# Kernel tuning notes

Measured on AMD Instinct MI355X. Metric: run time of the kernel, lower is better.

## Reference

```python
import jax, jax.numpy as jnp
import numpy as np

BATCH = 1024
A = 128  # image height
B = 128  # image width (must equal A for the original matmul chain to type-check)
N = 64   # attention grid size
H = 1024 # h_dim


def setup_inputs() -> dict:
    key = jax.random.key(0)
    k0, k1, k2, k3 = jax.random.split(key, 4)
    x = jax.random.normal(k0, (BATCH, A * B), dtype=jnp.float32)
    x_hat = jax.random.normal(k1, (BATCH, A * B), dtype=jnp.float32)
    h = jax.random.normal(k2, (BATCH, H), dtype=jnp.float32)
    W_read_w = jax.random.normal(k3, (5, H), dtype=jnp.float32) * 0.02
    W_read_b = jnp.zeros((5,), dtype=jnp.float32)
    return {"x": x, "x_hat": x_hat, "h": h, "W_read_w": W_read_w, "W_read_b": W_read_b}


def _compute_filterbanks(params):
    # params: (5,) from W_read(h)[0]
    gt_X, gt_Y, log_var, log_dt = params[0], params[1], params[2], params[3]
    var = jnp.exp(log_var + 1e-8)
    # .item() in the original detaches these from the autograd graph
    g_X = jax.lax.stop_gradient((A + 1) * (gt_X + 1) / 2)
    g_Y = jax.lax.stop_gradient((B + 1) * (gt_Y + 1) / 2)
    d = jax.lax.stop_gradient(jnp.exp(log_dt) * (max(A, B) - 1) / (N - 1))
    # linspace(g + (-N/2-0.5)d, g + (N-1-N/2-0.5)d, N) == g + (i - N/2 - 0.5)*d
    idx = jnp.arange(N, dtype=jnp.float32) - N / 2 - 0.5  # (N,)
    mu_X = g_X + idx * d  # (N,)
    mu_Y = g_Y + idx * d  # (N,)
    a = jnp.arange(A, dtype=jnp.float32)
    b = jnp.arange(B, dtype=jnp.float32)
    F_X = jnp.exp(-((a[None, :] - mu_X[:, None]) ** 2) / (2 * var))  # (N, A)
    F_Y = jnp.exp(-((b[None, :] - mu_Y[:, None]) ** 2) / (2 * var))  # (N, B)
    # NOTE: original normalizes by the GLOBAL sum, not per-row
    F_X = F_X / jnp.sum(F_X)
    F_Y = F_Y / jnp.sum(F_Y)
    return F_X, F_Y


def reference(x, x_hat, h, W_read_w, W_read_b):
    # params from FIRST batch element, shared across the whole batch (as in original)
    params = (h @ W_read_w.T + W_read_b)[0]  # (5,)
    gamma = jnp.exp(params[4])
    F_X, F_Y = _compute_filterbanks(params)  # (N,A), (N,B)

    xi = x.reshape(-1, A, B)
    xh = x_hat.reshape(-1, A, B)

    def filt(z):  # gamma * F_Y @ z @ F_X.T  -> (batch, N, N)
        t = jnp.einsum('na,kab->knb', F_Y, z)      # (batch, N, B)
        return gamma * jnp.einsum('knb,mb->knm', t, F_X)

    x_filt = filt(xi).reshape(-1, N * N)
    x_hat_filt = filt(xh).reshape(-1, N * N)
    return jnp.concatenate([x_filt, x_hat_filt], axis=1)  # (batch, 2*N*N)
```

## Files before the change

### kernel.cpp

```cpp
#include <hip/hip_runtime.h>
#include <math.h>

#define AB 128
#define NN 64
#define HD 1024

#define SFZ 256.0f
#define SFF 64.0f
#define DESCALE (1.0f / 1048576.0f)

typedef _Float16 half8 __attribute__((ext_vector_type(8)));
typedef float f32x4 __attribute__((ext_vector_type(4)));
typedef unsigned u32x4 __attribute__((ext_vector_type(4)));


__device__ __forceinline__ float wave_reduce(float v) {
  v += __shfl_down(v, 32);
  v += __shfl_down(v, 16);
  v += __shfl_down(v, 8);
  v += __shfl_down(v, 4);
  v += __shfl_down(v, 2);
  v += __shfl_down(v, 1);
  return v;
}

__global__ __launch_bounds__(1024) void fb_setup(
    const float* __restrict__ h, const float* __restrict__ Ww,
    const float* __restrict__ Wb, void* __restrict__ wsv) {
  __shared__ float redp[16][5];
  __shared__ float reds[16][2];
  __shared__ float sc[5];
  __shared__ float ssum[2];
  const int tid = threadIdx.x;
  const int lane = tid & 63;
  const int wv = tid >> 6;

  const float hv = h[tid];
  float p[5];
#pragma unroll
  for (int j = 0; j < 5; ++j) p[j] = hv * Ww[j * HD + tid];
#pragma unroll
  for (int j = 0; j < 5; ++j) {
    float r = wave_reduce(p[j]);
    if (lane == 0) redp[wv][j] = r;
  }
  __syncthreads();
  if (tid < 5) {
    float s = Wb[tid];
#pragma unroll
    for (int w = 0; w < 16; ++w) s += redp[w][tid];
    sc[tid] = s;
  }
  __syncthreads();

  const float gt_X = sc[0], gt_Y = sc[1], log_var = sc[2], log_dt = sc[3];
  const float var = expf(log_var + 1e-8f);
  const float g_X = (129.0f * (gt_X + 1.0f)) / 2.0f;
  const float g_Y = (129.0f * (gt_Y + 1.0f)) / 2.0f;
  const float d = (expf(log_dt) * 127.0f) / 63.0f;
  const float twovar = 2.0f * var;

  float fyv[8], fxv[8];
  float sY = 0.f, sX = 0.f;
#pragma unroll
  for (int c = 0; c < 8; ++c) {
    const int idx = tid + 1024 * c;
    const int n = idx >> 7;
    const int col = idx & 127;
    const float idxn = (float)n - 32.5f;
    const float muX = g_X + idxn * d;
    const float muY = g_Y + idxn * d;
    const float dx = (float)col - muX;
    const float dy = (float)col - muY;
    const float fx = expf(-(dx * dx) / twovar);
    const float fy = expf(-(dy * dy) / twovar);
    fyv[c] = fy;
    fxv[c] = fx;
    sY += fy;
    sX += fx;
  }
  {
    float rY = wave_reduce(sY);
    float rX = wave_reduce(sX);
    if (lane == 0) { reds[wv][0] = rY; reds[wv][1] = rX; }
  }
  __syncthreads();
  if (tid < 2) {
    float s = 0.f;
#pragma unroll
    for (int w = 0; w < 16; ++w) s += reds[w][tid];
    ssum[tid] = s;
  }
  __syncthreads();
  const float invY = 1.0f / ssum[0];
  const float invX = 1.0f / ssum[1];

  _Float16* FXhi = (_Float16*)wsv;
  _Float16* FXlo = FXhi + NN * AB;
  _Float16* FYhi = FXhi + 2 * NN * AB;
  _Float16* FYlo = FXhi + 3 * NN * AB;

#pragma unroll
  for (int c = 0; c < 8; ++c) {
    const int idx = tid + 1024 * c;
    const float vy = fyv[c] * invY * SFF;
    const float vx = fxv[c] * invX * SFF;
    const _Float16 yh = (_Float16)vy;
    const _Float16 xh2 = (_Float16)vx;
    FYhi[idx] = yh;
    FYlo[idx] = (_Float16)(vy - (float)yh);
    FXhi[idx] = xh2;
    FXlo[idx] = (_Float16)(vx - (float)xh2);
  }
  if (tid == 0) ((float*)wsv)[2 * NN * AB] = expf(sc[4]) * DESCALE;
}

__device__ __forceinline__ void split8(const f32x4 z0, const f32x4 z1,
                                       float s, half8& hi, half8& lo) {
#pragma unroll
  for (int e = 0; e < 8; ++e) {
    const float q = (e < 4 ? z0[e] : z1[e - 4]) * s;
    const _Float16 hh = (_Float16)q;
    hi[e] = hh;
    lo[e] = (_Float16)(q - (float)hh);
  }
}

__global__ __launch_bounds__(256) void fb_filt(
    const float* __restrict__ x, const float* __restrict__ xh,
    const void* __restrict__ wsv, float* __restrict__ out) {
  __shared__ unsigned S_lds[NN * 140];

  const int tid = threadIdx.x;
  const int lane = tid & 63;
  const int wv = tid >> 6;
  const int l15 = lane & 15;
  const int h4 = lane >> 4;
  const int bid = blockIdx.x;
  const int img = bid >> 1;
  const int which = bid & 1;
  const float* __restrict__ Z = (which ? xh : x) + (size_t)img * (AB * AB);
  const _Float16* __restrict__ FXhi = (const _Float16*)wsv;
  const _Float16* __restrict__ FXlo = FXhi + NN * AB;
  const _Float16* __restrict__ FYhi = FXhi + 2 * NN * AB;
  const _Float16* __restrict__ FYlo = FXhi + 3 * NN * AB;

  f32x4 acc[4][2];
#pragma unroll
  for (int mt = 0; mt < 4; ++mt)
#pragma unroll
    for (int j = 0; j < 2; ++j) acc[mt][j] = {0.f, 0.f, 0.f, 0.f};

#pragma unroll
  for (int ks = 0; ks < 4; ++ks) {
    half8 bhi[2], blo[2];
#pragma unroll
    for (int j = 0; j < 2; ++j) {
      const float* zp = Z + (32 * wv + 16 * j + l15) * AB + 32 * ks + 8 * h4;
      const f32x4 z0 = *(const f32x4*)zp;
      const f32x4 z1 = *(const f32x4*)(zp + 4);
      split8(z0, z1, SFZ, bhi[j], blo[j]);
    }
#pragma unroll
    for (int mt = 0; mt < 4; ++mt) {
      const int off = (16 * mt + l15) * AB + 32 * ks + 8 * h4;
      const half8 ahi = *(const half8*)(FXhi + off);
      const half8 alo = *(const half8*)(FXlo + off);
#pragma unroll
      for (int j = 0; j < 2; ++j) {
        acc[mt][j] = __builtin_amdgcn_mfma_f32_16x16x32_f16(ahi, bhi[j], acc[mt][j], 0, 0, 0);
        acc[mt][j] = __builtin_amdgcn_mfma_f32_16x16x32_f16(ahi, blo[j], acc[mt][j], 0, 0, 0);
        acc[mt][j] = __builtin_amdgcn_mfma_f32_16x16x32_f16(alo, bhi[j], acc[mt][j], 0, 0, 0);
      }
    }
  }

#pragma unroll
  for (int mt = 0; mt < 4; ++mt) {
#pragma unroll
    for (int j = 0; j < 2; ++j) {
      const int a = 32 * wv + 16 * j + l15;
#pragma unroll
      for (int r = 0; r < 4; ++r) {
        const float v = acc[mt][j][r];
        const _Float16 hh = (_Float16)v;
        const _Float16 ll = (_Float16)(v - (float)hh);
        const unsigned wpk =
            ((unsigned)__builtin_bit_cast(unsigned short, hh) << 16) |
            (unsigned)__builtin_bit_cast(unsigned short, ll);
        S_lds[(16 * mt + 4 * h4 + r) * 140 + a] = wpk;
      }
    }
  }
  __syncthreads();

  f32x4 acc2[4];
#pragma unroll
  for (int mt = 0; mt < 4; ++mt) acc2[mt] = {0.f, 0.f, 0.f, 0.f};

#pragma unroll
  for (int ks = 0; ks < 4; ++ks) {
    const int aoff = 32 * ks + 8 * h4;
    const int foff = (16 * wv + l15) * AB + aoff;
    const half8 ahi = *(const half8*)(FYhi + foff);
    const half8 alo = *(const half8*)(FYlo + foff);
#pragma unroll
    for (int mt = 0; mt < 4; ++mt) {
      const unsigned* sp = &S_lds[(16 * mt + l15) * 140 + aoff];
      const u32x4 w0 = *(const u32x4*)sp;
      const u32x4 w1 = *(const u32x4*)(sp + 4);
      u32x4 bhu, blu;
      bhu.x = __builtin_amdgcn_perm(w0.y, w0.x, 0x07060302u);
      blu.x = __builtin_amdgcn_perm(w0.y, w0.x, 0x05040100u);
      bhu.y = __builtin_amdgcn_perm(w0.w, w0.z, 0x07060302u);
      blu.y = __builtin_amdgcn_perm(w0.w, w0.z, 0x05040100u);
      bhu.z = __builtin_amdgcn_perm(w1.y, w1.x, 0x07060302u);
      blu.z = __builtin_amdgcn_perm(w1.y, w1.x, 0x05040100u);
      bhu.w = __builtin_amdgcn_perm(w1.w, w1.z, 0x07060302u);
      blu.w = __builtin_amdgcn_perm(w1.w, w1.z, 0x05040100u);
      const half8 bh = __builtin_bit_cast(half8, bhu);
      const half8 bl = __builtin_bit_cast(half8, blu);
      acc2[mt] = __builtin_amdgcn_mfma_f32_16x16x32_f16(ahi, bh, acc2[mt], 0, 0, 0);
      acc2[mt] = __builtin_amdgcn_mfma_f32_16x16x32_f16(ahi, bl, acc2[mt], 0, 0, 0);
      acc2[mt] = __builtin_amdgcn_mfma_f32_16x16x32_f16(alo, bh, acc2[mt], 0, 0, 0);
    }
  }

  const float gamma_eff = ((const float*)wsv)[2 * NN * AB];
  float* __restrict__ ob = out + (size_t)img * 8192 + which * 4096;
#pragma unroll
  for (int mt = 0; mt < 4; ++mt) {
#pragma unroll
    for (int r = 0; r < 4; ++r) {
      ob[(16 * wv + 4 * h4 + r) * 64 + 16 * mt + l15] = acc2[mt][r] * gamma_eff;
    }
  }
}

extern "C" void kernel_launch(void* const* d_in, const int* in_sizes, int n_in,
                              void* d_out, int out_size, void* d_ws, size_t ws_size,
                              hipStream_t stream) {
  const float* x = (const float*)d_in[0];
  const float* xh = (const float*)d_in[1];
  const float* h = (const float*)d_in[2];
  const float* Ww = (const float*)d_in[3];
  const float* Wb = (const float*)d_in[4];
  float* outp = (float*)d_out;

  fb_setup<<<1, 1024, 0, stream>>>(h, Ww, Wb, d_ws);
  fb_filt<<<2048, 256, 0, stream>>>(x, xh, (const void*)d_ws, outp);
}
```

Measured before the change: 195.2 us.

## Stage packed FX filterbank in swizzled LDS and prefetch image and FY operands

FX hi/lo halves are now packed into one 32-bit word per element in the workspace. Each block copies the packed array into an XOR-swizzled LDS buffer instead of every wave reading FX from global/L2 per k-step. Image loads are issued early and split around the LDS fill, FY fragments are preloaded into registers before the second GEMM, and stage-2 LDS reads are software-pipelined one tile ahead. The change adds a barrier and reuses the LDS buffer for both stages, raises register pressure with the launch_bounds occupancy hint, and relies on the swizzle to avoid bank conflicts that the old padding handled.

```diff
diff --git a/kernel.cpp b/kernel.cpp
--- a/kernel.cpp
+++ b/kernel.cpp
@@ -95,10 +95,9 @@
   const float invY = 1.0f / ssum[0];
   const float invX = 1.0f / ssum[1];
 
-  _Float16* FXhi = (_Float16*)wsv;
-  _Float16* FXlo = FXhi + NN * AB;
-  _Float16* FYhi = FXhi + 2 * NN * AB;
-  _Float16* FYlo = FXhi + 3 * NN * AB;
+  unsigned* FXp = (unsigned*)wsv;
+  _Float16* FYhi = (_Float16*)wsv + 2 * NN * AB;
+  _Float16* FYlo = FYhi + NN * AB;
 
 #pragma unroll
   for (int c = 0; c < 8; ++c) {
@@ -109,8 +108,9 @@
     const _Float16 xh2 = (_Float16)vx;
     FYhi[idx] = yh;
     FYlo[idx] = (_Float16)(vy - (float)yh);
-    FXhi[idx] = xh2;
-    FXlo[idx] = (_Float16)(vx - (float)xh2);
+    const _Float16 xl = (_Float16)(vx - (float)xh2);
+    FXp[idx] = ((unsigned)__builtin_bit_cast(unsigned short, xh2) << 16) |
+               (unsigned)__builtin_bit_cast(unsigned short, xl);
   }
   if (tid == 0) ((float*)wsv)[2 * NN * AB] = expf(sc[4]) * DESCALE;
 }
@@ -126,10 +126,25 @@
   }
 }
 
-__global__ __launch_bounds__(256) void fb_filt(
+__device__ __forceinline__ void unpack8(const u32x4 a0, const u32x4 a1,
+                                        half8& hi, half8& lo) {
+  u32x4 hu, lu;
+  hu.x = __builtin_amdgcn_perm(a0.y, a0.x, 0x07060302u);
+  lu.x = __builtin_amdgcn_perm(a0.y, a0.x, 0x05040100u);
+  hu.y = __builtin_amdgcn_perm(a0.w, a0.z, 0x07060302u);
+  lu.y = __builtin_amdgcn_perm(a0.w, a0.z, 0x05040100u);
+  hu.z = __builtin_amdgcn_perm(a1.y, a1.x, 0x07060302u);
+  lu.z = __builtin_amdgcn_perm(a1.y, a1.x, 0x05040100u);
+  hu.w = __builtin_amdgcn_perm(a1.w, a1.z, 0x07060302u);
+  lu.w = __builtin_amdgcn_perm(a1.w, a1.z, 0x05040100u);
+  hi = __builtin_bit_cast(half8, hu);
+  lo = __builtin_bit_cast(half8, lu);
+}
+
+__global__ __launch_bounds__(256, 4) void fb_filt(
     const float* __restrict__ x, const float* __restrict__ xh,
     const void* __restrict__ wsv, float* __restrict__ out) {
-  __shared__ unsigned S_lds[NN * 140];
+  __shared__ __align__(16) unsigned S_lds[NN * 128];
 
   const int tid = threadIdx.x;
   const int lane = tid & 63;
@@ -140,10 +155,44 @@
   const int img = bid >> 1;
   const int which = bid & 1;
   const float* __restrict__ Z = (which ? xh : x) + (size_t)img * (AB * AB);
-  const _Float16* __restrict__ FXhi = (const _Float16*)wsv;
-  const _Float16* __restrict__ FXlo = FXhi + NN * AB;
-  const _Float16* __restrict__ FYhi = FXhi + 2 * NN * AB;
-  const _Float16* __restrict__ FYlo = FXhi + 3 * NN * AB;
+  const unsigned* __restrict__ FXp = (const unsigned*)wsv;
+  const _Float16* __restrict__ FYhi = (const _Float16*)wsv + 2 * NN * AB;
+  const _Float16* __restrict__ FYlo = FYhi + NN * AB;
+  const float gamma_eff = ((const float*)wsv)[2 * NN * AB];
+
+  const float* __restrict__ zrow = Z + (32 * wv + l15) * AB + 8 * h4;
+  f32x4 z[4][4];
+#pragma unroll
+  for (int ks = 0; ks < 2; ++ks) {
+    const float* p0 = zrow + 32 * ks;
+    const float* p1 = zrow + 16 * AB + 32 * ks;
+    z[ks][0] = *(const f32x4*)p0;
+    z[ks][1] = *(const f32x4*)(p0 + 4);
+    z[ks][2] = *(const f32x4*)p1;
+    z[ks][3] = *(const f32x4*)(p1 + 4);
+  }
+  {
+    const int swc = 4 * ((tid >> 5) & 7);
+    const int colw = (tid * 4) & 127;
+    const int rbase = tid >> 5;
+#pragma unroll
+    for (int c = 0; c < 8; ++c) {
+      const u32x4 v = *(const u32x4*)(FXp + c * 1024 + tid * 4);
+      *(u32x4*)&S_lds[(c * 8 + rbase) * 128 + (colw ^ swc)] = v;
+    }
+  }
+  __syncthreads();
+
+#pragma unroll
+  for (int ks = 2; ks < 4; ++ks) {
+    const float* p0 = zrow + 32 * ks;
+    const float* p1 = zrow + 16 * AB + 32 * ks;
+    z[ks][0] = *(const f32x4*)p0;
+    z[ks][1] = *(const f32x4*)(p0 + 4);
+    z[ks][2] = *(const f32x4*)p1;
+    z[ks][3] = *(const f32x4*)(p1 + 4);
+  }
+  __builtin_amdgcn_sched_barrier(0);
 
   f32x4 acc[4][2];
 #pragma unroll
@@ -151,21 +200,20 @@
 #pragma unroll
     for (int j = 0; j < 2; ++j) acc[mt][j] = {0.f, 0.f, 0.f, 0.f};
 
+  const int sw1 = 4 * (l15 & 7);
 #pragma unroll
   for (int ks = 0; ks < 4; ++ks) {
     half8 bhi[2], blo[2];
-#pragma unroll
-    for (int j = 0; j < 2; ++j) {
-      const float* zp = Z + (32 * wv + 16 * j + l15) * AB + 32 * ks + 8 * h4;
-      const f32x4 z0 = *(const f32x4*)zp;
-      const f32x4 z1 = *(const f32x4*)(zp + 4);
-      split8(z0, z1, SFZ, bhi[j], blo[j]);
-    }
+    split8(z[ks][0], z[ks][1], SFZ, bhi[0], blo[0]);
+    split8(z[ks][2], z[ks][3], SFZ, bhi[1], blo[1]);
+    const int c0 = (32 * ks + 8 * h4) ^ sw1;
 #pragma unroll
     for (int mt = 0; mt < 4; ++mt) {
-      const int off = (16 * mt + l15) * AB + 32 * ks + 8 * h4;
-      const half8 ahi = *(const half8*)(FXhi + off);
-      const half8 alo = *(const half8*)(FXlo + off);
+      const int base = (16 * mt + l15) * 128;
+      const u32x4 a0 = *(const u32x4*)&S_lds[base + c0];
+      const u32x4 a1 = *(const u32x4*)&S_lds[base + (c0 ^ 4)];
+      half8 ahi, alo;
+      unpack8(a0, a1, ahi, alo);
 #pragma unroll
       for (int j = 0; j < 2; ++j) {
         acc[mt][j] = __builtin_amdgcn_mfma_f32_16x16x32_f16(ahi, bhi[j], acc[mt][j], 0, 0, 0);
@@ -174,6 +222,7 @@
       }
     }
   }
+  __syncthreads();
 
 #pragma unroll
   for (int mt = 0; mt < 4; ++mt) {
@@ -182,51 +231,55 @@
       const int a = 32 * wv + 16 * j + l15;
 #pragma unroll
       for (int r = 0; r < 4; ++r) {
+        const int row = 16 * mt + 4 * h4 + r;
         const float v = acc[mt][j][r];
         const _Float16 hh = (_Float16)v;
         const _Float16 ll = (_Float16)(v - (float)hh);
         const unsigned wpk =
             ((unsigned)__builtin_bit_cast(unsigned short, hh) << 16) |
             (unsigned)__builtin_bit_cast(unsigned short, ll);
-        S_lds[(16 * mt + 4 * h4 + r) * 140 + a] = wpk;
+        S_lds[row * 128 + ((a >> 2) * 4 ^ (4 * (row & 7))) + (a & 3)] = wpk;
       }
     }
   }
+
+  half8 fyh[4], fyl[4];
+#pragma unroll
+  for (int ks = 0; ks < 4; ++ks) {
+    const int foff = (16 * wv + l15) * AB + 32 * ks + 8 * h4;
+    fyh[ks] = *(const half8*)(FYhi + foff);
+    fyl[ks] = *(const half8*)(FYlo + foff);
+  }
+  __builtin_amdgcn_sched_barrier(0);
   __syncthreads();
 
   f32x4 acc2[4];
 #pragma unroll
   for (int mt = 0; mt < 4; ++mt) acc2[mt] = {0.f, 0.f, 0.f, 0.f};
 
+  const int sw2 = 4 * (l15 & 7);
 #pragma unroll
   for (int ks = 0; ks < 4; ++ks) {
-    const int aoff = 32 * ks + 8 * h4;
-    const int foff = (16 * wv + l15) * AB + aoff;
-    const half8 ahi = *(const half8*)(FYhi + foff);
-    const half8 alo = *(const half8*)(FYlo + foff);
+    const int c0 = (32 * ks + 8 * h4) ^ sw2;
+    u32x4 w0 = *(const u32x4*)&S_lds[l15 * 128 + c0];
+    u32x4 w1 = *(const u32x4*)&S_lds[l15 * 128 + (c0 ^ 4)];
 #pragma unroll
     for (int mt = 0; mt < 4; ++mt) {
-      const unsigned* sp = &S_lds[(16 * mt + l15) * 140 + aoff];
-      const u32x4 w0 = *(const u32x4*)sp;
-      const u32x4 w1 = *(const u32x4*)(sp + 4);
-      u32x4 bhu, blu;
-      bhu.x = __builtin_amdgcn_perm(w0.y, w0.x, 0x07060302u);
-      blu.x = __builtin_amdgcn_perm(w0.y, w0.x, 0x05040100u);
-      bhu.y = __builtin_amdgcn_perm(w0.w, w0.z, 0x07060302u);
-      blu.y = __builtin_amdgcn_perm(w0.w, w0.z, 0x05040100u);
-      bhu.z = __builtin_amdgcn_perm(w1.y, w1.x, 0x07060302u);
-      blu.z = __builtin_amdgcn_perm(w1.y, w1.x, 0x05040100u);
-      bhu.w = __builtin_amdgcn_perm(w1.w, w1.z, 0x07060302u);
-      blu.w = __builtin_amdgcn_perm(w1.w, w1.z, 0x05040100u);
-      const half8 bh = __builtin_bit_cast(half8, bhu);
-      const half8 bl = __builtin_bit_cast(half8, blu);
-      acc2[mt] = __builtin_amdgcn_mfma_f32_16x16x32_f16(ahi, bh, acc2[mt], 0, 0, 0);
-      acc2[mt] = __builtin_amdgcn_mfma_f32_16x16x32_f16(ahi, bl, acc2[mt], 0, 0, 0);
-      acc2[mt] = __builtin_amdgcn_mfma_f32_16x16x32_f16(alo, bh, acc2[mt], 0, 0, 0);
-    }
-  }
-
-  const float gamma_eff = ((const float*)wsv)[2 * NN * AB];
+      u32x4 n0, n1;
+      if (mt < 3) {
+        const int base2 = (16 * (mt + 1) + l15) * 128;
+        n0 = *(const u32x4*)&S_lds[base2 + c0];
+        n1 = *(const u32x4*)&S_lds[base2 + (c0 ^ 4)];
+      }
+      half8 bh, bl;
+      unpack8(w0, w1, bh, bl);
+      acc2[mt] = __builtin_amdgcn_mfma_f32_16x16x32_f16(fyh[ks], bh, acc2[mt], 0, 0, 0);
+      acc2[mt] = __builtin_amdgcn_mfma_f32_16x16x32_f16(fyh[ks], bl, acc2[mt], 0, 0, 0);
+      acc2[mt] = __builtin_amdgcn_mfma_f32_16x16x32_f16(fyl[ks], bh, acc2[mt], 0, 0, 0);
+      if (mt < 3) { w0 = n0; w1 = n1; }
+    }
+  }
+
   float* __restrict__ ob = out + (size_t)img * 8192 + which * 4096;
 #pragma unroll
   for (int mt = 0; mt < 4; ++mt) {
```

New measurement: 176.0 us. 9.8% less time.
